# Kernel tuning notes

Hardware: AMD Instinct MI355X
Metric: run time of the kernel (lower is better)

## Reference

```python
import jax, jax.numpy as jnp
import numpy as np
import math

NUM_IN_C = 128      # rep_2d num_c (c_z)
ATT_C = 64          # attention_num_c
NUM_HEADS = 4
B, T, I, J = 1, 4, 256, 256


def setup_inputs() -> dict:
    key = jax.random.key(0)
    ks = jax.random.split(key, 7)
    s = 1.0 / math.sqrt(NUM_IN_C)
    return {
        "z2d": jax.random.normal(ks[0], (B, I, J, NUM_IN_C), dtype=jnp.float32),
        "t2d": jax.random.normal(ks[1], (B, T, I, J, NUM_IN_C), dtype=jnp.float32),
        # nn.Linear weights are [out_features, in_features]; apply as x @ W.T
        "Wq": jax.random.normal(ks[2], (ATT_C * NUM_HEADS, NUM_IN_C), dtype=jnp.float32) * s,
        "Wk": jax.random.normal(ks[3], (ATT_C * NUM_HEADS, NUM_IN_C), dtype=jnp.float32) * s,
        "Wv": jax.random.normal(ks[4], (ATT_C * NUM_HEADS, NUM_IN_C), dtype=jnp.float32) * s,
        "Wo": jax.random.normal(ks[5], (NUM_IN_C, ATT_C * NUM_HEADS), dtype=jnp.float32) * s,
        "bo": jax.random.normal(ks[6], (NUM_IN_C,), dtype=jnp.float32) * 0.02,
    }


def reference(z2d, t2d, Wq, Wk, Wv, Wo, bo):
    # Projections; reshape last dim to (attention_num_c, num_heads) per torch .view
    q = (z2d @ Wq.T).reshape(*z2d.shape[:-1], ATT_C, NUM_HEADS)        # b i j c h
    k = (t2d @ Wk.T).reshape(*t2d.shape[:-1], ATT_C, NUM_HEADS)        # b t i j c h
    v = (t2d @ Wv.T).reshape(*t2d.shape[:-1], ATT_C, NUM_HEADS)        # b t i j c h
    # NOTE: original scales by sqrt(num_in_c), not sqrt(attention_num_c)
    scores = jnp.einsum('bijch,btijch->btijh', q, k) / math.sqrt(NUM_IN_C)
    w = jax.nn.softmax(scores, axis=1)                                  # softmax over template axis t
    out = jnp.einsum('btijh,btijch->bijch', w, v)                       # b i j c h
    out = out.reshape(*out.shape[:-2], ATT_C * NUM_HEADS)               # flatten (c,h)
    return out @ Wo.T + bo
```

## Files before the change

kernel.cpp:

```cpp
#include <hip/hip_runtime.h>


#define PIX 65536

typedef __attribute__((ext_vector_type(8))) short s8v;
typedef __attribute__((ext_vector_type(4))) float f4v;
typedef __attribute__((ext_vector_type(4))) unsigned int u4v;
typedef __attribute__((ext_vector_type(4))) float fl4;

__device__ __forceinline__ unsigned short f2bf(float x) {
    unsigned int u = __float_as_uint(x);
    u = (u + 0x7FFFu + ((u >> 16) & 1u)) >> 16;
    return (unsigned short)u;
}
__device__ __forceinline__ float bf2fs(short v) {
    return __uint_as_float(((unsigned int)(unsigned short)v) << 16);
}

__global__ __launch_bounds__(256) void build_weights(
        const float* __restrict__ Wq, const float* __restrict__ Wk,
        const float* __restrict__ Wv, const float* __restrict__ Wo,
        unsigned short* __restrict__ mcat, unsigned short* __restrict__ pcat) {
    int b = blockIdx.x;
    if (b < 256) {
        int idx = b * 256 + threadIdx.x;
        int n = idx >> 7, k1 = idx & 127;
        int h = n >> 7, k2 = n & 127;
        float s = 0.f;
        #pragma unroll 8
        for (int c = 0; c < 64; c++) {
            int r = c * 4 + h;
            s += Wq[r * 128 + k1] * Wk[r * 128 + k2];
        }
        mcat[idx] = f2bf(s * 0.088388347648318447f);
    } else {
        int idx = (b - 256) * 256 + threadIdx.x;
        int m = idx >> 9, kk = idx & 511;
        int h = kk >> 7, k = kk & 127;
        float s = 0.f;
        #pragma unroll 8
        for (int c = 0; c < 64; c++) {
            int r = c * 4 + h;
            s += Wo[m * 256 + r] * Wv[r * 128 + k];
        }
        pcat[idx] = f2bf(s);
    }
}

#define S_SCR_OFS (512 * 136)
#define S_USH (S_SCR_OFS + 8 * 16 * 72)

__global__ __launch_bounds__(512, 2) void score_kernel(
    const float* __restrict__ z2d, const float* __restrict__ t2d,
    const unsigned short* __restrict__ mcat, float* __restrict__ wbuf) {

    __shared__ unsigned short sm[S_USH];
    const int tid = threadIdx.x;

    #pragma unroll
    for (int i = 0; i < 16; i++) {
        int g8 = i * 512 + tid;
        int row = g8 >> 4, c8 = g8 & 15;
        *(u4v*)&sm[row * 136 + c8 * 8] = *(const u4v*)(mcat + (size_t)g8 * 8);
    }
    __syncthreads();

    const int wv = tid >> 6, lane = tid & 63, quad = lane >> 4, l15 = lane & 15;
    unsigned short* scr = &sm[S_SCR_OFS + wv * (16 * 72)];

    for (int it = 0; it < 2; it++) {
        const int p0 = blockIdx.x * 256 + (wv * 2 + it) * 16;

        s8v za[4];
        {
            const float* zp = z2d + (size_t)(p0 + l15) * 128 + quad * 8;
            #pragma unroll
            for (int ks = 0; ks < 4; ks++) {
                const fl4 d0 = *(const fl4*)(zp + ks * 32);
                const fl4 d1 = *(const fl4*)(zp + ks * 32 + 4);
                s8v a;
                a[0] = (short)f2bf(d0[0]); a[1] = (short)f2bf(d0[1]);
                a[2] = (short)f2bf(d0[2]); a[3] = (short)f2bf(d0[3]);
                a[4] = (short)f2bf(d1[0]); a[5] = (short)f2bf(d1[1]);
                a[6] = (short)f2bf(d1[2]); a[7] = (short)f2bf(d1[3]);
                za[ks] = a;
            }
        }
        s8v atf[4][4];
        #pragma unroll
        for (int t = 0; t < 4; t++) {
            const float* ap = t2d + ((size_t)t * PIX + p0 + l15) * 128 + quad * 8;
            #pragma unroll
            for (int kf = 0; kf < 4; kf++) {
                const fl4 d0 = *(const fl4*)(ap + kf * 32);
                const fl4 d1 = *(const fl4*)(ap + kf * 32 + 4);
                s8v a;
                a[0] = (short)f2bf(d0[0]); a[1] = (short)f2bf(d0[1]);
                a[2] = (short)f2bf(d0[2]); a[3] = (short)f2bf(d0[3]);
                a[4] = (short)f2bf(d1[0]); a[5] = (short)f2bf(d1[1]);
                a[6] = (short)f2bf(d1[2]); a[7] = (short)f2bf(d1[3]);
                atf[t][kf] = a;
            }
        }

        for (int h = 0; h < 4; h++) {
            f4v dac[4];
            #pragma unroll
            for (int t = 0; t < 4; t++) dac[t] = (f4v){0.f, 0.f, 0.f, 0.f};

            #pragma unroll
            for (int ph = 0; ph < 2; ph++) {
                f4v uacc[4];
                #pragma unroll
                for (int c = 0; c < 4; c++) {
                    const int brow = h * 128 + (ph * 4 + c) * 16 + l15;
                    f4v acc = {0.f, 0.f, 0.f, 0.f};
                    #pragma unroll
                    for (int ks = 0; ks < 4; ks++) {
                        const s8v b = *(const s8v*)&sm[brow * 136 + ks * 32 + quad * 8];
                        acc = __builtin_amdgcn_mfma_f32_16x16x32_bf16(za[ks], b, acc, 0, 0, 0);
                    }
                    uacc[c] = acc;
                }
                #pragma unroll
                for (int c = 0; c < 4; c++)
                    #pragma unroll
                    for (int r = 0; r < 4; r++)
                        scr[(quad * 4 + r) * 72 + c * 16 + l15] = f2bf(uacc[c][r]);
                __threadfence_block();
                #pragma unroll
                for (int ks2 = 0; ks2 < 2; ks2++) {
                    const s8v uf = *(const s8v*)&scr[l15 * 72 + ks2 * 32 + quad * 8];
                    const int kf = ph * 2 + ks2;
                    #pragma unroll
                    for (int t = 0; t < 4; t++)
                        dac[t] = __builtin_amdgcn_mfma_f32_16x16x32_bf16(
                            uf, atf[t][kf], dac[t], 0, 0, 0);
                }
                __threadfence_block();
            }
            if ((l15 >> 2) == quad) {
                const int r = l15 & 3;
                float x0 = r == 0 ? dac[0][0] : r == 1 ? dac[0][1] : r == 2 ? dac[0][2] : dac[0][3];
                float x1 = r == 0 ? dac[1][0] : r == 1 ? dac[1][1] : r == 2 ? dac[1][2] : dac[1][3];
                float x2 = r == 0 ? dac[2][0] : r == 1 ? dac[2][1] : r == 2 ? dac[2][2] : dac[2][3];
                float x3 = r == 0 ? dac[3][0] : r == 1 ? dac[3][1] : r == 2 ? dac[3][2] : dac[3][3];
                float mx = fmaxf(fmaxf(x0, x1), fmaxf(x2, x3));
                float e0 = __expf(x0 - mx), e1 = __expf(x1 - mx);
                float e2 = __expf(x2 - mx), e3 = __expf(x3 - mx);
                float inv = 1.f / (e0 + e1 + e2 + e3);
                float* wp = wbuf + (size_t)h * 4 * PIX + p0 + l15;
                wp[0 * PIX] = e0 * inv; wp[1 * PIX] = e1 * inv;
                wp[2 * PIX] = e2 * inv; wp[3 * PIX] = e3 * inv;
            }
        }
    }
}

#define O_USH (128 * 520)

__global__ __launch_bounds__(512, 2) void out_kernel(
    const float* __restrict__ t2d, const unsigned short* __restrict__ pcat,
    const float* __restrict__ wbuf, const float* __restrict__ bo,
    float* __restrict__ out) {

    __shared__ unsigned short sm[O_USH];
    const int tid = threadIdx.x;

    #pragma unroll
    for (int i = 0; i < 16; i++) {
        int g8 = i * 512 + tid;
        int row = g8 >> 6, c8 = g8 & 63;
        *(u4v*)&sm[row * 520 + c8 * 8] = *(const u4v*)(pcat + (size_t)g8 * 8);
    }
    __syncthreads();

    const int wv = tid >> 6, lane = tid & 63, quad = lane >> 4, l15 = lane & 15;
    const int p0 = blockIdx.x * 256 + wv * 32;

    float wgt[4][2][4];
    #pragma unroll
    for (int h = 0; h < 4; h++)
        #pragma unroll
        for (int t = 0; t < 4; t++)
            #pragma unroll
            for (int mt = 0; mt < 2; mt++)
                wgt[t][mt][h] = wbuf[(size_t)(h * 4 + t) * PIX + p0 + mt * 16 + l15];

    f4v acc[2][8];
    #pragma unroll
    for (int mt = 0; mt < 2; mt++)
        #pragma unroll
        for (int ct = 0; ct < 8; ct++) acc[mt][ct] = (f4v){0.f, 0.f, 0.f, 0.f};

    #pragma unroll
    for (int ks = 0; ks < 4; ks++) {
        s8v ab[4][2];
        #pragma unroll
        for (int t = 0; t < 4; t++)
            #pragma unroll
            for (int mt = 0; mt < 2; mt++) {
                const float* ap = t2d + ((size_t)t * PIX + p0 + mt * 16 + l15) * 128
                                  + ks * 32 + quad * 8;
                const fl4 d0 = *(const fl4*)ap;
                const fl4 d1 = *(const fl4*)(ap + 4);
                s8v a;
                a[0] = (short)f2bf(d0[0]); a[1] = (short)f2bf(d0[1]);
                a[2] = (short)f2bf(d0[2]); a[3] = (short)f2bf(d0[3]);
                a[4] = (short)f2bf(d1[0]); a[5] = (short)f2bf(d1[1]);
                a[6] = (short)f2bf(d1[2]); a[7] = (short)f2bf(d1[3]);
                ab[t][mt] = a;
            }
        #pragma unroll
        for (int h = 0; h < 4; h++) {
            s8v af[2];
            #pragma unroll
            for (int mt = 0; mt < 2; mt++) {
                s8v o;
                #pragma unroll
                for (int j = 0; j < 8; j++) {
                    float v = wgt[0][mt][h] * bf2fs(ab[0][mt][j])
                            + wgt[1][mt][h] * bf2fs(ab[1][mt][j])
                            + wgt[2][mt][h] * bf2fs(ab[2][mt][j])
                            + wgt[3][mt][h] * bf2fs(ab[3][mt][j]);
                    o[j] = (short)f2bf(v);
                }
                af[mt] = o;
            }
            #pragma unroll
            for (int ct = 0; ct < 8; ct++) {
                const s8v b = *(const s8v*)&sm[(ct * 16 + l15) * 520
                                               + h * 128 + ks * 32 + quad * 8];
                acc[0][ct] = __builtin_amdgcn_mfma_f32_16x16x32_bf16(af[0], b, acc[0][ct], 0, 0, 0);
                acc[1][ct] = __builtin_amdgcn_mfma_f32_16x16x32_bf16(af[1], b, acc[1][ct], 0, 0, 0);
            }
        }
    }

    #pragma unroll
    for (int ct = 0; ct < 8; ct++) {
        const float bb = bo[ct * 16 + l15];
        #pragma unroll
        for (int mt = 0; mt < 2; mt++)
            #pragma unroll
            for (int r = 0; r < 4; r++)
                out[(size_t)(p0 + mt * 16 + quad * 4 + r) * 128 + ct * 16 + l15]
                    = acc[mt][ct][r] + bb;
    }
}

extern "C" void kernel_launch(void* const* d_in, const int* in_sizes, int n_in,
                              void* d_out, int out_size, void* d_ws, size_t ws_size,
                              hipStream_t stream) {
    const float* z2d = (const float*)d_in[0];
    const float* t2d = (const float*)d_in[1];
    const float* Wq  = (const float*)d_in[2];
    const float* Wk  = (const float*)d_in[3];
    const float* Wv  = (const float*)d_in[4];
    const float* Wo  = (const float*)d_in[5];
    const float* bo  = (const float*)d_in[6];

    unsigned short* mcat = (unsigned short*)d_ws;
    unsigned short* pcat = mcat + 512 * 128;
    float* wbuf = (float*)(pcat + 128 * 512);

    build_weights<<<512, 256, 0, stream>>>(Wq, Wk, Wv, Wo, mcat, pcat);
    score_kernel<<<256, 512, 0, stream>>>(z2d, t2d, mcat, wbuf);
    out_kernel<<<256, 512, 0, stream>>>(t2d, pcat, wbuf, bo, (float*)d_out);
}
```

Before: 277.4 us.

## Restructure score and output kernels with per-head LDS staging and smaller blocks

Both main kernels are rewritten. Blocks shrink to 256 threads with 1024 blocks, and each head's weight slice is staged in XOR-swizzled shared memory instead of loading the whole matrix once. The score kernel now computes the second contraction with scalar FMAs plus shuffle reductions instead of an LDS scratch round-trip through a second MFMA. The output kernel mixes templates in fp32 before a single bf16 conversion. Conversions use the hardware packed bf16 instruction. The changes aim to cut LDS traffic, register pressure and conversion cost and to raise occupancy, at the cost of more syncthreads and repeated weight loads per block.

```diff
diff --git a/kernel.cpp b/kernel.cpp
--- a/kernel.cpp
+++ b/kernel.cpp
@@ -13,9 +13,24 @@
     u = (u + 0x7FFFu + ((u >> 16) & 1u)) >> 16;
     return (unsigned short)u;
 }
-__device__ __forceinline__ float bf2fs(short v) {
-    return __uint_as_float(((unsigned int)(unsigned short)v) << 16);
-}
+
+__device__ __forceinline__ unsigned int cvtpk(float lo, float hi) {
+    unsigned int r;
+    asm("v_cvt_pk_bf16_f32 %0, %1, %2" : "=v"(r) : "v"(lo), "v"(hi));
+    return r;
+}
+
+__device__ __forceinline__ s8v pack8(fl4 d0, fl4 d1) {
+    union { u4v u; s8v s; } cv;
+    cv.u[0] = cvtpk(d0[0], d0[1]);
+    cv.u[1] = cvtpk(d0[2], d0[3]);
+    cv.u[2] = cvtpk(d1[0], d1[1]);
+    cv.u[3] = cvtpk(d1[2], d1[3]);
+    return cv.s;
+}
+
+__device__ __forceinline__ float bflo(unsigned int u) { return __uint_as_float(u << 16); }
+__device__ __forceinline__ float bfhi(unsigned int u) { return __uint_as_float(u & 0xffff0000u); }
 
 __global__ __launch_bounds__(256) void build_weights(
         const float* __restrict__ Wq, const float* __restrict__ Wk,
@@ -47,205 +62,162 @@
     }
 }
 
-#define S_SCR_OFS (512 * 136)
-#define S_USH (S_SCR_OFS + 8 * 16 * 72)
-
-__global__ __launch_bounds__(512, 2) void score_kernel(
+__global__ __launch_bounds__(256, 3) void score_kernel(
     const float* __restrict__ z2d, const float* __restrict__ t2d,
     const unsigned short* __restrict__ mcat, float* __restrict__ wbuf) {
 
-    __shared__ unsigned short sm[S_USH];
+    __shared__ unsigned short sm[128 * 128];
     const int tid = threadIdx.x;
-
-    #pragma unroll
-    for (int i = 0; i < 16; i++) {
-        int g8 = i * 512 + tid;
-        int row = g8 >> 4, c8 = g8 & 15;
-        *(u4v*)&sm[row * 136 + c8 * 8] = *(const u4v*)(mcat + (size_t)g8 * 8);
-    }
-    __syncthreads();
-
     const int wv = tid >> 6, lane = tid & 63, quad = lane >> 4, l15 = lane & 15;
-    unsigned short* scr = &sm[S_SCR_OFS + wv * (16 * 72)];
-
-    for (int it = 0; it < 2; it++) {
-        const int p0 = blockIdx.x * 256 + (wv * 2 + it) * 16;
-
-        s8v za[4];
-        {
-            const float* zp = z2d + (size_t)(p0 + l15) * 128 + quad * 8;
+    const int p = blockIdx.x * 64 + wv * 16 + l15;
+
+    s8v za[4];
+    {
+        const float* zp = z2d + (size_t)p * 128 + quad * 8;
+        #pragma unroll
+        for (int ks = 0; ks < 4; ks++)
+            za[ks] = pack8(*(const fl4*)(zp + ks * 32), *(const fl4*)(zp + ks * 32 + 4));
+    }
+    unsigned int a2[4][8][2];
+    #pragma unroll
+    for (int t = 0; t < 4; t++) {
+        const float* ap = t2d + ((size_t)t * PIX + p) * 128 + quad * 4;
+        #pragma unroll
+        for (int cb = 0; cb < 8; cb++) {
+            const fl4 v = *(const fl4*)(ap + cb * 16);
+            a2[t][cb][0] = cvtpk(v[0], v[1]);
+            a2[t][cb][1] = cvtpk(v[2], v[3]);
+        }
+    }
+
+    for (int h = 0; h < 4; h++) {
+        __syncthreads();
+        #pragma unroll
+        for (int i = 0; i < 8; i++) {
+            const int g8 = i * 256 + tid;
+            const int row = g8 >> 4, c8 = g8 & 15;
+            *(u4v*)&sm[row * 128 + ((c8 ^ (row & 7)) * 8)] =
+                *(const u4v*)(mcat + (size_t)(h * 128 + row) * 128 + c8 * 8);
+        }
+        __syncthreads();
+
+        float ps[4] = {0.f, 0.f, 0.f, 0.f};
+        #pragma unroll
+        for (int cb = 0; cb < 8; cb++) {
+            f4v u = {0.f, 0.f, 0.f, 0.f};
             #pragma unroll
             for (int ks = 0; ks < 4; ks++) {
-                const fl4 d0 = *(const fl4*)(zp + ks * 32);
-                const fl4 d1 = *(const fl4*)(zp + ks * 32 + 4);
-                s8v a;
-                a[0] = (short)f2bf(d0[0]); a[1] = (short)f2bf(d0[1]);
-                a[2] = (short)f2bf(d0[2]); a[3] = (short)f2bf(d0[3]);
-                a[4] = (short)f2bf(d1[0]); a[5] = (short)f2bf(d1[1]);
-                a[6] = (short)f2bf(d1[2]); a[7] = (short)f2bf(d1[3]);
-                za[ks] = a;
-            }
-        }
-        s8v atf[4][4];
+                const s8v a = *(const s8v*)&sm[(cb * 16 + l15) * 128 +
+                                               (((ks * 4 + quad) ^ (l15 & 7)) * 8)];
+                u = __builtin_amdgcn_mfma_f32_16x16x32_bf16(a, za[ks], u, 0, 0, 0);
+            }
+            #pragma unroll
+            for (int t = 0; t < 4; t++) {
+                const float a0 = bflo(a2[t][cb][0]), a1 = bfhi(a2[t][cb][0]);
+                const float b0 = bflo(a2[t][cb][1]), b1 = bfhi(a2[t][cb][1]);
+                ps[t] += u[0] * a0 + u[1] * a1 + u[2] * b0 + u[3] * b1;
+            }
+        }
         #pragma unroll
         for (int t = 0; t < 4; t++) {
-            const float* ap = t2d + ((size_t)t * PIX + p0 + l15) * 128 + quad * 8;
-            #pragma unroll
-            for (int kf = 0; kf < 4; kf++) {
-                const fl4 d0 = *(const fl4*)(ap + kf * 32);
-                const fl4 d1 = *(const fl4*)(ap + kf * 32 + 4);
-                s8v a;
-                a[0] = (short)f2bf(d0[0]); a[1] = (short)f2bf(d0[1]);
-                a[2] = (short)f2bf(d0[2]); a[3] = (short)f2bf(d0[3]);
-                a[4] = (short)f2bf(d1[0]); a[5] = (short)f2bf(d1[1]);
-                a[6] = (short)f2bf(d1[2]); a[7] = (short)f2bf(d1[3]);
-                atf[t][kf] = a;
-            }
-        }
-
-        for (int h = 0; h < 4; h++) {
-            f4v dac[4];
-            #pragma unroll
-            for (int t = 0; t < 4; t++) dac[t] = (f4v){0.f, 0.f, 0.f, 0.f};
-
-            #pragma unroll
-            for (int ph = 0; ph < 2; ph++) {
-                f4v uacc[4];
-                #pragma unroll
-                for (int c = 0; c < 4; c++) {
-                    const int brow = h * 128 + (ph * 4 + c) * 16 + l15;
-                    f4v acc = {0.f, 0.f, 0.f, 0.f};
-                    #pragma unroll
-                    for (int ks = 0; ks < 4; ks++) {
-                        const s8v b = *(const s8v*)&sm[brow * 136 + ks * 32 + quad * 8];
-                        acc = __builtin_amdgcn_mfma_f32_16x16x32_bf16(za[ks], b, acc, 0, 0, 0);
-                    }
-                    uacc[c] = acc;
-                }
-                #pragma unroll
-                for (int c = 0; c < 4; c++)
-                    #pragma unroll
-                    for (int r = 0; r < 4; r++)
-                        scr[(quad * 4 + r) * 72 + c * 16 + l15] = f2bf(uacc[c][r]);
-                __threadfence_block();
-                #pragma unroll
-                for (int ks2 = 0; ks2 < 2; ks2++) {
-                    const s8v uf = *(const s8v*)&scr[l15 * 72 + ks2 * 32 + quad * 8];
-                    const int kf = ph * 2 + ks2;
-                    #pragma unroll
-                    for (int t = 0; t < 4; t++)
-                        dac[t] = __builtin_amdgcn_mfma_f32_16x16x32_bf16(
-                            uf, atf[t][kf], dac[t], 0, 0, 0);
-                }
-                __threadfence_block();
-            }
-            if ((l15 >> 2) == quad) {
-                const int r = l15 & 3;
-                float x0 = r == 0 ? dac[0][0] : r == 1 ? dac[0][1] : r == 2 ? dac[0][2] : dac[0][3];
-                float x1 = r == 0 ? dac[1][0] : r == 1 ? dac[1][1] : r == 2 ? dac[1][2] : dac[1][3];
-                float x2 = r == 0 ? dac[2][0] : r == 1 ? dac[2][1] : r == 2 ? dac[2][2] : dac[2][3];
-                float x3 = r == 0 ? dac[3][0] : r == 1 ? dac[3][1] : r == 2 ? dac[3][2] : dac[3][3];
-                float mx = fmaxf(fmaxf(x0, x1), fmaxf(x2, x3));
-                float e0 = __expf(x0 - mx), e1 = __expf(x1 - mx);
-                float e2 = __expf(x2 - mx), e3 = __expf(x3 - mx);
-                float inv = 1.f / (e0 + e1 + e2 + e3);
-                float* wp = wbuf + (size_t)h * 4 * PIX + p0 + l15;
-                wp[0 * PIX] = e0 * inv; wp[1 * PIX] = e1 * inv;
-                wp[2 * PIX] = e2 * inv; wp[3 * PIX] = e3 * inv;
-            }
-        }
-    }
-}
-
-#define O_USH (128 * 520)
-
-__global__ __launch_bounds__(512, 2) void out_kernel(
+            ps[t] += __shfl_xor(ps[t], 16);
+            ps[t] += __shfl_xor(ps[t], 32);
+        }
+        const float mx = fmaxf(fmaxf(ps[0], ps[1]), fmaxf(ps[2], ps[3]));
+        float e[4], sum = 0.f;
+        #pragma unroll
+        for (int t = 0; t < 4; t++) { e[t] = __expf(ps[t] - mx); sum += e[t]; }
+        const float inv = 1.f / sum;
+        if (quad == 0) {
+            #pragma unroll
+            for (int t = 0; t < 4; t++)
+                wbuf[(size_t)(h * 4 + t) * PIX + p] = e[t] * inv;
+        }
+    }
+}
+
+__global__ __launch_bounds__(256, 3) void out_kernel(
     const float* __restrict__ t2d, const unsigned short* __restrict__ pcat,
     const float* __restrict__ wbuf, const float* __restrict__ bo,
     float* __restrict__ out) {
 
-    __shared__ unsigned short sm[O_USH];
+    __shared__ unsigned short sm[128 * 128];
     const int tid = threadIdx.x;
-
-    #pragma unroll
-    for (int i = 0; i < 16; i++) {
-        int g8 = i * 512 + tid;
-        int row = g8 >> 6, c8 = g8 & 63;
-        *(u4v*)&sm[row * 520 + c8 * 8] = *(const u4v*)(pcat + (size_t)g8 * 8);
-    }
-    __syncthreads();
-
     const int wv = tid >> 6, lane = tid & 63, quad = lane >> 4, l15 = lane & 15;
-    const int p0 = blockIdx.x * 256 + wv * 32;
-
-    float wgt[4][2][4];
+    const int p0 = blockIdx.x * 64 + wv * 16;
+    const int p = p0 + l15;
+
+    float wgt[4][4];
     #pragma unroll
     for (int h = 0; h < 4; h++)
         #pragma unroll
         for (int t = 0; t < 4; t++)
-            #pragma unroll
-            for (int mt = 0; mt < 2; mt++)
-                wgt[t][mt][h] = wbuf[(size_t)(h * 4 + t) * PIX + p0 + mt * 16 + l15];
-
-    f4v acc[2][8];
-    #pragma unroll
-    for (int mt = 0; mt < 2; mt++)
-        #pragma unroll
-        for (int ct = 0; ct < 8; ct++) acc[mt][ct] = (f4v){0.f, 0.f, 0.f, 0.f};
-
-    #pragma unroll
-    for (int ks = 0; ks < 4; ks++) {
-        s8v ab[4][2];
-        #pragma unroll
-        for (int t = 0; t < 4; t++)
-            #pragma unroll
-            for (int mt = 0; mt < 2; mt++) {
-                const float* ap = t2d + ((size_t)t * PIX + p0 + mt * 16 + l15) * 128
-                                  + ks * 32 + quad * 8;
-                const fl4 d0 = *(const fl4*)ap;
-                const fl4 d1 = *(const fl4*)(ap + 4);
-                s8v a;
-                a[0] = (short)f2bf(d0[0]); a[1] = (short)f2bf(d0[1]);
-                a[2] = (short)f2bf(d0[2]); a[3] = (short)f2bf(d0[3]);
-                a[4] = (short)f2bf(d1[0]); a[5] = (short)f2bf(d1[1]);
-                a[6] = (short)f2bf(d1[2]); a[7] = (short)f2bf(d1[3]);
-                ab[t][mt] = a;
-            }
+            wgt[h][t] = wbuf[(size_t)(h * 4 + t) * PIX + p];
+
+    s8v af[4][4];
+    #pragma unroll
+    for (int kf = 0; kf < 4; kf++) {
+        float f[4][8];
+        #pragma unroll
+        for (int h = 0; h < 4; h++)
+            #pragma unroll
+            for (int j = 0; j < 8; j++) f[h][j] = 0.f;
+        #pragma unroll
+        for (int t = 0; t < 4; t++) {
+            const float* ap = t2d + ((size_t)t * PIX + p) * 128 + kf * 32 + quad * 8;
+            const fl4 d0 = *(const fl4*)ap;
+            const fl4 d1 = *(const fl4*)(ap + 4);
+            #pragma unroll
+            for (int h = 0; h < 4; h++) {
+                const float w = wgt[h][t];
+                #pragma unroll
+                for (int j = 0; j < 4; j++) {
+                    f[h][j]     += w * d0[j];
+                    f[h][j + 4] += w * d1[j];
+                }
+            }
+        }
         #pragma unroll
         for (int h = 0; h < 4; h++) {
-            s8v af[2];
-            #pragma unroll
-            for (int mt = 0; mt < 2; mt++) {
-                s8v o;
-                #pragma unroll
-                for (int j = 0; j < 8; j++) {
-                    float v = wgt[0][mt][h] * bf2fs(ab[0][mt][j])
-                            + wgt[1][mt][h] * bf2fs(ab[1][mt][j])
-                            + wgt[2][mt][h] * bf2fs(ab[2][mt][j])
-                            + wgt[3][mt][h] * bf2fs(ab[3][mt][j]);
-                    o[j] = (short)f2bf(v);
-                }
-                af[mt] = o;
-            }
+            union { u4v u; s8v s; } cv;
+            cv.u[0] = cvtpk(f[h][0], f[h][1]);
+            cv.u[1] = cvtpk(f[h][2], f[h][3]);
+            cv.u[2] = cvtpk(f[h][4], f[h][5]);
+            cv.u[3] = cvtpk(f[h][6], f[h][7]);
+            af[h][kf] = cv.s;
+        }
+    }
+
+    f4v acc[8];
+    #pragma unroll
+    for (int ct = 0; ct < 8; ct++) acc[ct] = (f4v){0.f, 0.f, 0.f, 0.f};
+
+    for (int h = 0; h < 4; h++) {
+        __syncthreads();
+        #pragma unroll
+        for (int i = 0; i < 8; i++) {
+            const int g8 = i * 256 + tid;
+            const int row = g8 >> 4, c8 = g8 & 15;
+            *(u4v*)&sm[row * 128 + ((c8 ^ (row & 7)) * 8)] =
+                *(const u4v*)(pcat + (size_t)row * 512 + h * 128 + c8 * 8);
+        }
+        __syncthreads();
+        #pragma unroll
+        for (int kf = 0; kf < 4; kf++)
             #pragma unroll
             for (int ct = 0; ct < 8; ct++) {
-                const s8v b = *(const s8v*)&sm[(ct * 16 + l15) * 520
-                                               + h * 128 + ks * 32 + quad * 8];
-                acc[0][ct] = __builtin_amdgcn_mfma_f32_16x16x32_bf16(af[0], b, acc[0][ct], 0, 0, 0);
-                acc[1][ct] = __builtin_amdgcn_mfma_f32_16x16x32_bf16(af[1], b, acc[1][ct], 0, 0, 0);
-            }
-        }
+                const s8v b = *(const s8v*)&sm[(ct * 16 + l15) * 128 +
+                                               (((kf * 4 + quad) ^ (l15 & 7)) * 8)];
+                acc[ct] = __builtin_amdgcn_mfma_f32_16x16x32_bf16(af[h][kf], b, acc[ct], 0, 0, 0);
+            }
     }
 
     #pragma unroll
     for (int ct = 0; ct < 8; ct++) {
         const float bb = bo[ct * 16 + l15];
         #pragma unroll
-        for (int mt = 0; mt < 2; mt++)
-            #pragma unroll
-            for (int r = 0; r < 4; r++)
-                out[(size_t)(p0 + mt * 16 + quad * 4 + r) * 128 + ct * 16 + l15]
-                    = acc[mt][ct][r] + bb;
+        for (int r = 0; r < 4; r++)
+            out[(size_t)(p0 + quad * 4 + r) * 128 + ct * 16 + l15] = acc[ct][r] + bb;
     }
 }
 
@@ -265,6 +237,6 @@
     float* wbuf = (float*)(pcat + 128 * 512);
 
     build_weights<<<512, 256, 0, stream>>>(Wq, Wk, Wv, Wo, mcat, pcat);
-    score_kernel<<<256, 512, 0, stream>>>(z2d, t2d, mcat, wbuf);
-    out_kernel<<<256, 512, 0, stream>>>(t2d, pcat, wbuf, bo, (float*)d_out);
-}
+    score_kernel<<<1024, 256, 0, stream>>>(z2d, t2d, mcat, wbuf);
+    out_kernel<<<1024, 256, 0, stream>>>(t2d, pcat, wbuf, bo, (float*)d_out);
+}
```

Measured after the change: 312.3 us. 12.6% more time.
